# Kernel optimization log

Hardware: AMD Instinct MI355X
Metric: run time of the kernel (lower is better)

## Reference

```python
import jax, jax.numpy as jnp
import numpy as np


def fwht(x):
    """Fast Walsh-Hadamard transform along the last axis (unnormalized)."""
    orig_shape = x.shape
    n = orig_shape[-1]
    x = x.reshape(-1, n)
    h = 1
    while h < n:
        x = x.reshape(-1, n // (2 * h), 2, h)
        a = x[:, :, 0, :]
        b = x[:, :, 1, :]
        x = jnp.stack([a + b, a - b], axis=2).reshape(-1, n)
        h *= 2
    return x.reshape(orig_shape)


def setup_inputs() -> dict:
    key = jax.random.key(0)
    ks = jax.random.split(key, 8)
    M, N = 16384, 4096          # m_pad (out), n_pad (in), powers of 2
    T = 8192
    CB = 65536                  # E8 codebook entries (int16 index space)
    x = jax.random.normal(ks[0], (T, N), dtype=jnp.float32)
    Qidxs = jax.random.randint(ks[1], (M, N // 8), 0, CB, dtype=jnp.int32)
    Qidxs2 = jax.random.randint(ks[2], (M, N // 8), 0, CB, dtype=jnp.int32)
    SU = jnp.where(jax.random.uniform(ks[3], (M,)) < 0.5, -1.0, 1.0).astype(jnp.float32)
    SV = jnp.where(jax.random.uniform(ks[4], (N,)) < 0.5, -1.0, 1.0).astype(jnp.float32)
    codebook = jax.random.normal(ks[5], (CB, 8), dtype=jnp.float32)
    codebook2 = jax.random.normal(ks[6], (CB, 8), dtype=jnp.float32)
    Wscale = jnp.array([0.02], dtype=jnp.float32)
    inv_resid_scale = jnp.array([0.25], dtype=jnp.float32)
    return {"x": x, "Qidxs": Qidxs, "Qidxs2": Qidxs2, "SU": SU, "SV": SV,
            "codebook": codebook, "codebook2": codebook2,
            "Wscale": Wscale, "inv_resid_scale": inv_resid_scale}


def reference(x, Qidxs, Qidxs2, SU, SV, codebook, codebook2, Wscale, inv_resid_scale):
    M = Qidxs.shape[0]
    N = Qidxs.shape[1] * 8
    inv_sqrt_n = 1.0 / np.sqrt(N).astype(np.float32)
    inv_sqrt_m = 1.0 / np.sqrt(M).astype(np.float32)
    # Dequantize RHT-domain weight: 2 residual stages of E8 codebook lookups.
    W_hat = codebook[Qidxs].reshape(M, N)                      # (M, N)
    W_hat = W_hat + inv_resid_scale * codebook2[Qidxs2].reshape(M, N)
    # Input-side RHT: sign flip then normalized Hadamard.
    t = fwht(x * SV) * inv_sqrt_n                              # (T, N)
    # GEMM in the transformed domain.
    z = t @ W_hat.T                                            # (T, M)
    # Output-side RHT: normalized Hadamard, sign flip, global scale.
    y = (fwht(z) * inv_sqrt_m) * SU * Wscale                   # (T, M)
    return y
```

## Files before the change

### kernel.cpp

```cpp
#include <hip/hip_runtime.h>
#include <stdint.h>


typedef __attribute__((ext_vector_type(8)))  __bf16 bf16x8;
typedef __attribute__((ext_vector_type(4)))  float  f32x4;
typedef __attribute__((ext_vector_type(4)))  unsigned short us4;
typedef __attribute__((ext_vector_type(8)))  unsigned short us8;

#define T_ROWS 8192
#define N_DIM  4096
#define M_DIM  16384

__device__ __forceinline__ unsigned short f2bf(float f) {
    unsigned int u = __float_as_uint(f);
    u = (u + 0x7FFFu + ((u >> 16) & 1u)) >> 16;
    return (unsigned short)u;
}
__device__ __forceinline__ float bf2f(unsigned short h) {
    return __uint_as_float(((unsigned int)h) << 16);
}

__device__ __forceinline__ void g2l16(const void* g, void* l) {
    __builtin_amdgcn_global_load_lds(
        (const __attribute__((address_space(1))) void*)g,
        (__attribute__((address_space(3))) void*)l,
        16, 0, 0);
}

__device__ __forceinline__ void fwht16(float v[16]) {
#pragma unroll
    for (int h = 1; h < 16; h <<= 1) {
#pragma unroll
        for (int g = 0; g < 16; g += 2 * h) {
#pragma unroll
            for (int k = 0; k < h; ++k) {
                float a = v[g + k], b = v[g + k + h];
                v[g + k]     = a + b;
                v[g + k + h] = a - b;
            }
        }
    }
}

__device__ __forceinline__ void fwht8(float v[8]) {
#pragma unroll
    for (int h = 1; h < 8; h <<= 1) {
#pragma unroll
        for (int g = 0; g < 8; g += 2 * h) {
#pragma unroll
            for (int k = 0; k < h; ++k) {
                float a = v[g + k], b = v[g + k + h];
                v[g + k]     = a + b;
                v[g + k + h] = a - b;
            }
        }
    }
}

__global__ __launch_bounds__(256) void fwht_x_kernel(
    const float* __restrict__ x, const float* __restrict__ SV,
    unsigned short* __restrict__ t)
{
    __shared__ float s1[16 * 257];
    __shared__ float s2[256 * 17];
    const int row = blockIdx.x;
    const int tid = threadIdx.x;
    float v[16];

    const float4* xv  = (const float4*)(x + (size_t)row * N_DIM + tid * 16);
    const float4* svv = (const float4*)(SV + tid * 16);
#pragma unroll
    for (int q = 0; q < 4; ++q) {
        float4 a = xv[q], b = svv[q];
        v[q*4+0] = a.x*b.x; v[q*4+1] = a.y*b.y;
        v[q*4+2] = a.z*b.z; v[q*4+3] = a.w*b.w;
    }
    fwht16(v);
#pragma unroll
    for (int c = 0; c < 16; ++c) s1[c * 257 + tid] = v[c];
    __syncthreads();

    {
        const int a = tid >> 4, c = tid & 15;
        const float* base = &s1[c * 257 + a * 16];
#pragma unroll
        for (int b = 0; b < 16; ++b) v[b] = base[b];
        fwht16(v);
#pragma unroll
        for (int b = 0; b < 16; ++b) s2[(b * 16 + c) * 17 + a] = v[b];
    }
    __syncthreads();

    {
        const float* base = &s2[tid * 17];
#pragma unroll
        for (int a = 0; a < 16; ++a) v[a] = base[a];
        fwht16(v);
        const float sc = 1.0f / 64.0f;
        unsigned short* out = t + (size_t)row * N_DIM + tid;
#pragma unroll
        for (int a = 0; a < 16; ++a) out[a * 256] = f2bf(v[a] * sc);
    }
}

__device__ __forceinline__ void fwht128_tile(float* __restrict__ s, int tid)
{
#pragma unroll
    for (int k = 0; k < 2; ++k) {
        int sA = tid + k * 256;
        int c = sA & 63, a = sA >> 6;
        float* base = s + c * 129 + a * 16;
        float v[16];
#pragma unroll
        for (int j = 0; j < 16; ++j) v[j] = base[j];
        fwht16(v);
#pragma unroll
        for (int j = 0; j < 16; ++j) base[j] = v[j];
    }
    __syncthreads();
#pragma unroll
    for (int k = 0; k < 4; ++k) {
        int sB = tid + k * 256;
        int c = sB & 63, j = sB >> 6;
        float* base = s + c * 129 + j;
        float v[8];
#pragma unroll
        for (int a = 0; a < 8; ++a) v[a] = base[a * 16];
        fwht8(v);
#pragma unroll
        for (int a = 0; a < 8; ++a) base[a * 16] = v[a];
    }
    __syncthreads();
}

__global__ __launch_bounds__(256) void dec_fwht_kernel(
    const int* __restrict__ Qidxs, const int* __restrict__ Qidxs2,
    const float* __restrict__ cb, const float* __restrict__ cb2,
    const float* __restrict__ inv_resid_scale,
    unsigned short* __restrict__ W)
{
    __shared__ float s[64 * 129];
    const int nt  = blockIdx.x;
    const int grp = blockIdx.y;
    const int tid = threadIdx.x;
    const float irs = inv_resid_scale[0];

#pragma unroll
    for (int k = 0; k < 4; ++k) {
        int slot = tid + k * 256;
        int r = slot >> 3, e = slot & 7;
        size_t m = (size_t)grp * 128 + r;
        size_t q = m * (N_DIM / 8) + nt * 8 + e;
        int i1 = Qidxs[q], i2 = Qidxs2[q];
        const float4* c1 = (const float4*)(cb  + (size_t)i1 * 8);
        const float4* c2 = (const float4*)(cb2 + (size_t)i2 * 8);
        float4 a0 = c1[0], a1 = c1[1], b0 = c2[0], b1 = c2[1];
        float* col = s + (e * 8) * 129 + r;
        col[0 * 129] = a0.x + irs * b0.x;
        col[1 * 129] = a0.y + irs * b0.y;
        col[2 * 129] = a0.z + irs * b0.z;
        col[3 * 129] = a0.w + irs * b0.w;
        col[4 * 129] = a1.x + irs * b1.x;
        col[5 * 129] = a1.y + irs * b1.y;
        col[6 * 129] = a1.z + irs * b1.z;
        col[7 * 129] = a1.w + irs * b1.w;
    }
    __syncthreads();

    fwht128_tile(s, tid);

#pragma unroll
    for (int k = 0; k < 4; ++k) {
        int slot = tid + k * 256;
        int r = slot >> 3, e = slot & 7;
        size_t m = (size_t)grp * 128 + r;
        const float* col = s + (e * 8) * 129 + r;
        us8 o;
#pragma unroll
        for (int j = 0; j < 8; ++j) o[j] = f2bf(col[j * 129]);
        *(us8*)(W + m * N_DIM + nt * 64 + e * 8) = o;
    }
}

__global__ __launch_bounds__(256) void colfwht2_kernel(
    unsigned short* __restrict__ W)
{
    __shared__ float s[64 * 129];
    const int nt  = blockIdx.x;
    const int grp = blockIdx.y;
    const int tid = threadIdx.x;

#pragma unroll
    for (int k = 0; k < 4; ++k) {
        int slot = tid + k * 256;
        int r = slot >> 3, e = slot & 7;
        size_t m = (size_t)grp + (size_t)r * 128;
        us8 v = *(const us8*)(W + m * N_DIM + nt * 64 + e * 8);
        float* col = s + (e * 8) * 129 + r;
#pragma unroll
        for (int j = 0; j < 8; ++j) col[j * 129] = bf2f(v[j]);
    }
    __syncthreads();

    fwht128_tile(s, tid);

    const float sc = 1.0f / 128.0f;
#pragma unroll
    for (int k = 0; k < 4; ++k) {
        int slot = tid + k * 256;
        int r = slot >> 3, e = slot & 7;
        size_t m = (size_t)grp + (size_t)r * 128;
        const float* col = s + (e * 8) * 129 + r;
        us8 o;
#pragma unroll
        for (int j = 0; j < 8; ++j) o[j] = f2bf(col[j * 129] * sc);
        *(us8*)(W + m * N_DIM + nt * 64 + e * 8) = o;
    }
}

__global__ __launch_bounds__(256) void gemm_kernel(
    const unsigned short* __restrict__ A,
    const unsigned short* __restrict__ B,
    const float* __restrict__ SU,
    const float* __restrict__ Wscale,
    float* __restrict__ Y)
{
    __shared__ unsigned short As[128 * 32];
    __shared__ unsigned short Bs[128 * 32];

    const int tid  = threadIdx.x;
    const int lane = tid & 63;
    const int w    = tid >> 6;
    const int wm   = w & 1;
    const int wn   = w >> 1;
    const int i0   = blockIdx.x * 128;
    const int j0   = blockIdx.y * 128;

    f32x4 acc[4][4] = {};

    const int lrow = lane >> 2;
    const int lc8  = (lane & 3) * 8;

    for (int k0 = 0; k0 < N_DIM; k0 += 32) {
        __syncthreads();
#pragma unroll
        for (int q = 0; q < 2; ++q) {
            const int rr = w * 32 + q * 16;
            const unsigned short* ga =
                A + (size_t)(i0 + rr + lrow) * N_DIM + k0 + lc8;
            g2l16(ga, &As[rr * 32]);
            const unsigned short* gb =
                B + (size_t)(j0 + rr + lrow) * N_DIM + k0 + lc8;
            g2l16(gb, &Bs[rr * 32]);
        }
        __syncthreads();

        const int k8   = (lane >> 4) * 8;
        const int mrow = lane & 15;
        bf16x8 af[4], bfr[4];
#pragma unroll
        for (int tm = 0; tm < 4; ++tm)
            af[tm] = *(const bf16x8*)&As[(wm * 64 + tm * 16 + mrow) * 32 + k8];
#pragma unroll
        for (int tn = 0; tn < 4; ++tn)
            bfr[tn] = *(const bf16x8*)&Bs[(wn * 64 + tn * 16 + mrow) * 32 + k8];
#pragma unroll
        for (int tm = 0; tm < 4; ++tm)
#pragma unroll
            for (int tn = 0; tn < 4; ++tn)
                acc[tm][tn] = __builtin_amdgcn_mfma_f32_16x16x32_bf16(
                    af[tm], bfr[tn], acc[tm][tn], 0, 0, 0);
    }

    const float wsc  = Wscale[0];
    const int ccol  = lane & 15;
    const int crow4 = (lane >> 4) * 4;
#pragma unroll
    for (int tn = 0; tn < 4; ++tn) {
        const int col = j0 + wn * 64 + tn * 16 + ccol;
        const float su = SU[col] * wsc;
#pragma unroll
        for (int tm = 0; tm < 4; ++tm) {
            const int rowb = i0 + wm * 64 + tm * 16 + crow4;
#pragma unroll
            for (int r = 0; r < 4; ++r)
                Y[(size_t)(rowb + r) * M_DIM + col] = acc[tm][tn][r] * su;
        }
    }
}

extern "C" void kernel_launch(void* const* d_in, const int* in_sizes, int n_in,
                              void* d_out, int out_size, void* d_ws, size_t ws_size,
                              hipStream_t stream) {
    const float* x       = (const float*)d_in[0];
    const int*   Qidxs   = (const int*)  d_in[1];
    const int*   Qidxs2  = (const int*)  d_in[2];
    const float* SU      = (const float*)d_in[3];
    const float* SV      = (const float*)d_in[4];
    const float* cb      = (const float*)d_in[5];
    const float* cb2     = (const float*)d_in[6];
    const float* Wscale  = (const float*)d_in[7];
    const float* irs     = (const float*)d_in[8];
    float*       y       = (float*)d_out;

    char* ws = (char*)d_ws;
    unsigned short* t  = (unsigned short*)ws;
    unsigned short* W1 = (unsigned short*)(ws + ((size_t)64 << 20));

    fwht_x_kernel<<<T_ROWS, 256, 0, stream>>>(x, SV, t);
    dec_fwht_kernel<<<dim3(N_DIM / 64, M_DIM / 128), 256, 0, stream>>>(
        Qidxs, Qidxs2, cb, cb2, irs, W1);
    colfwht2_kernel<<<dim3(N_DIM / 64, M_DIM / 128), 256, 0, stream>>>(W1);
    gemm_kernel<<<dim3(T_ROWS / 128, M_DIM / 128), 256, 0, stream>>>(
        t, W1, SU, Wscale, y);
}
```

Measured before the change: 2.076 ms.

## Rewrite GEMM as 256x256 tiles with double-buffered swizzled LDS pipeline

Replaces the simple 128x128 GEMM, which reloaded a 32-wide K slice with two syncthreads per step, with a 512-thread 256x256 block tile over 64-wide K tiles. Global-to-LDS loads are double-buffered and issued ahead, with waitcnt-controlled prefetch. LDS uses an XOR swizzle to avoid bank conflicts, and MFMA phases are interleaved with barriers and setprio. The aim is to raise arithmetic intensity and hide memory latency behind the matrix math. The cost is 128KB of LDS per block and many more accumulators per thread, which limits occupancy and adds register pressure.

```diff
diff --git a/kernel.cpp b/kernel.cpp
--- a/kernel.cpp
+++ b/kernel.cpp
@@ -10,6 +10,7 @@
 #define T_ROWS 8192
 #define N_DIM  4096
 #define M_DIM  16384
+#define NT_TILES 64
 
 __device__ __forceinline__ unsigned short f2bf(float f) {
     unsigned int u = __float_as_uint(f);
@@ -218,73 +219,164 @@
     }
 }
 
-__global__ __launch_bounds__(256) void gemm_kernel(
+__global__ __launch_bounds__(512, 2) void gemm_kernel(
     const unsigned short* __restrict__ A,
     const unsigned short* __restrict__ B,
     const float* __restrict__ SU,
     const float* __restrict__ Wscale,
     float* __restrict__ Y)
 {
-    __shared__ unsigned short As[128 * 32];
-    __shared__ unsigned short Bs[128 * 32];
+    __shared__ unsigned short lds[65536];
+    char* ldsc = (char*)lds;
 
     const int tid  = threadIdx.x;
     const int lane = tid & 63;
     const int w    = tid >> 6;
-    const int wm   = w & 1;
-    const int wn   = w >> 1;
-    const int i0   = blockIdx.x * 128;
-    const int j0   = blockIdx.y * 128;
-
-    f32x4 acc[4][4] = {};
-
-    const int lrow = lane >> 2;
-    const int lc8  = (lane & 3) * 8;
-
-    for (int k0 = 0; k0 < N_DIM; k0 += 32) {
-        __syncthreads();
-#pragma unroll
-        for (int q = 0; q < 2; ++q) {
-            const int rr = w * 32 + q * 16;
-            const unsigned short* ga =
-                A + (size_t)(i0 + rr + lrow) * N_DIM + k0 + lc8;
-            g2l16(ga, &As[rr * 32]);
-            const unsigned short* gb =
-                B + (size_t)(j0 + rr + lrow) * N_DIM + k0 + lc8;
-            g2l16(gb, &Bs[rr * 32]);
+    const int wm   = w >> 2;
+    const int wn   = w & 3;
+    const int i0   = blockIdx.x * 256;
+    const int j0   = blockIdx.y * 256;
+
+    const int kgl = lane >> 4;
+    const int lr  = lane & 15;
+    const int rA0 = wm * 128 + lr;
+    const int rB0 = wn * 64  + lr;
+    const int baseA = rA0 * 64 + (kgl ^ ((rA0 >> 1) & 3)) * 16;
+    const int baseB = rB0 * 64 + (kgl ^ ((rB0 >> 1) & 3)) * 16;
+
+    const int G0  = w * 64 + lane;
+    const int G1  = G0 + 512;
+    const int r0g = G0 >> 2, r1g = G1 >> 2;
+    const int kg0 = (G0 & 3) ^ ((r0g >> 1) & 3);
+    const int kg1 = (G1 & 3) ^ ((r1g >> 1) & 3);
+    const unsigned short* Asrc0 = A + (size_t)(i0 + r0g) * N_DIM + kg0 * 8;
+    const unsigned short* Asrc1 = A + (size_t)(i0 + r1g) * N_DIM + kg1 * 8;
+    const unsigned short* Bsrc0 = B + (size_t)(j0 + r0g) * N_DIM + kg0 * 8;
+    const unsigned short* Bsrc1 = B + (size_t)(j0 + r1g) * N_DIM + kg1 * 8;
+    const int ldst0 = G0 * 16 - lane * 16;
+    const int ldst1 = ldst0 + 8192;
+
+    f32x4 acc[8][4] = {};
+
+    g2l16(Asrc0 +  0, ldsc + 0             + ldst0);
+    g2l16(Asrc1 +  0, ldsc + 0             + ldst1);
+    g2l16(Bsrc0 +  0, ldsc + 32768         + ldst0);
+    g2l16(Bsrc1 +  0, ldsc + 32768         + ldst1);
+    g2l16(Asrc0 + 32, ldsc + 16384         + ldst0);
+    g2l16(Asrc1 + 32, ldsc + 16384         + ldst1);
+    g2l16(Bsrc0 + 32, ldsc + 32768 + 16384 + ldst0);
+    g2l16(Bsrc1 + 32, ldsc + 32768 + 16384 + ldst1);
+    g2l16(Asrc0 + 64, ldsc + 65536         + ldst0);
+    g2l16(Asrc1 + 64, ldsc + 65536         + ldst1);
+    g2l16(Bsrc0 + 64, ldsc + 65536 + 32768 + ldst0);
+    g2l16(Bsrc1 + 64, ldsc + 65536 + 32768 + ldst1);
+    asm volatile("s_waitcnt vmcnt(4)" ::: "memory");
+    __builtin_amdgcn_s_barrier();
+
+#pragma unroll 1
+    for (int ktp = 0; ktp < NT_TILES; ktp += 2) {
+#pragma unroll
+        for (int p = 0; p < 2; ++p) {
+            const int  kt  = ktp + p;
+            const int  k0  = kt * 64;
+            const int  sp  = p * 65536;
+            const int  so  = (1 - p) * 65536;
+            const bool st1 = (kt + 1) < NT_TILES;
+            const bool st2 = (kt + 2) < NT_TILES;
+
+            bf16x8 a[8], c[8], b0, b1, b2, b3, d0, d1, d2, d3;
+
+#pragma unroll
+            for (int mf = 0; mf < 8; ++mf)
+                a[mf] = *(const bf16x8*)(ldsc + sp + baseA + mf * 1024);
+            b0 = *(const bf16x8*)(ldsc + sp + 32768 + baseB + 0 * 1024);
+            b1 = *(const bf16x8*)(ldsc + sp + 32768 + baseB + 1 * 1024);
+            if (st1) {
+                g2l16(Asrc0 + k0 + 96, ldsc + so + 16384 + ldst0);
+                g2l16(Asrc1 + k0 + 96, ldsc + so + 16384 + ldst1);
+            }
+            __builtin_amdgcn_s_barrier();
+            __builtin_amdgcn_s_setprio(1);
+#pragma unroll
+            for (int mf = 0; mf < 8; ++mf) {
+                acc[mf][0] = __builtin_amdgcn_mfma_f32_16x16x32_bf16(a[mf], b0, acc[mf][0], 0, 0, 0);
+                acc[mf][1] = __builtin_amdgcn_mfma_f32_16x16x32_bf16(a[mf], b1, acc[mf][1], 0, 0, 0);
+            }
+            __builtin_amdgcn_s_setprio(0);
+            __builtin_amdgcn_s_barrier();
+
+            b2 = *(const bf16x8*)(ldsc + sp + 32768 + baseB + 2 * 1024);
+            b3 = *(const bf16x8*)(ldsc + sp + 32768 + baseB + 3 * 1024);
+#pragma unroll
+            for (int mf = 0; mf < 4; ++mf)
+                c[mf] = *(const bf16x8*)(ldsc + sp + 16384 + baseA + mf * 1024);
+            if (st1) {
+                g2l16(Bsrc0 + k0 + 96, ldsc + so + 32768 + 16384 + ldst0);
+                g2l16(Bsrc1 + k0 + 96, ldsc + so + 32768 + 16384 + ldst1);
+            }
+            __builtin_amdgcn_s_barrier();
+            __builtin_amdgcn_s_setprio(1);
+#pragma unroll
+            for (int mf = 0; mf < 8; ++mf) {
+                acc[mf][2] = __builtin_amdgcn_mfma_f32_16x16x32_bf16(a[mf], b2, acc[mf][2], 0, 0, 0);
+                acc[mf][3] = __builtin_amdgcn_mfma_f32_16x16x32_bf16(a[mf], b3, acc[mf][3], 0, 0, 0);
+            }
+            __builtin_amdgcn_s_setprio(0);
+            __builtin_amdgcn_s_barrier();
+
+#pragma unroll
+            for (int mf = 4; mf < 8; ++mf)
+                c[mf] = *(const bf16x8*)(ldsc + sp + 16384 + baseA + mf * 1024);
+            d0 = *(const bf16x8*)(ldsc + sp + 32768 + 16384 + baseB + 0 * 1024);
+            d1 = *(const bf16x8*)(ldsc + sp + 32768 + 16384 + baseB + 1 * 1024);
+            if (st2) {
+                g2l16(Asrc0 + k0 + 128, ldsc + sp + ldst0);
+                g2l16(Asrc1 + k0 + 128, ldsc + sp + ldst1);
+            }
+            __builtin_amdgcn_s_barrier();
+            __builtin_amdgcn_s_setprio(1);
+#pragma unroll
+            for (int mf = 0; mf < 8; ++mf) {
+                acc[mf][0] = __builtin_amdgcn_mfma_f32_16x16x32_bf16(c[mf], d0, acc[mf][0], 0, 0, 0);
+                acc[mf][1] = __builtin_amdgcn_mfma_f32_16x16x32_bf16(c[mf], d1, acc[mf][1], 0, 0, 0);
+            }
+            __builtin_amdgcn_s_setprio(0);
+            __builtin_amdgcn_s_barrier();
+
+            d2 = *(const bf16x8*)(ldsc + sp + 32768 + 16384 + baseB + 2 * 1024);
+            d3 = *(const bf16x8*)(ldsc + sp + 32768 + 16384 + baseB + 3 * 1024);
+            if (st2) {
+                g2l16(Bsrc0 + k0 + 128, ldsc + sp + 32768 + ldst0);
+                g2l16(Bsrc1 + k0 + 128, ldsc + sp + 32768 + ldst1);
+                asm volatile("s_waitcnt vmcnt(4)" ::: "memory");
+            } else {
+                asm volatile("s_waitcnt vmcnt(0)" ::: "memory");
+            }
+            __builtin_amdgcn_s_barrier();
+            __builtin_amdgcn_s_setprio(1);
+#pragma unroll
+            for (int mf = 0; mf < 8; ++mf) {
+                acc[mf][2] = __builtin_amdgcn_mfma_f32_16x16x32_bf16(c[mf], d2, acc[mf][2], 0, 0, 0);
+                acc[mf][3] = __builtin_amdgcn_mfma_f32_16x16x32_bf16(c[mf], d3, acc[mf][3], 0, 0, 0);
+            }
+            __builtin_amdgcn_s_setprio(0);
+            __builtin_amdgcn_s_barrier();
         }
-        __syncthreads();
-
-        const int k8   = (lane >> 4) * 8;
-        const int mrow = lane & 15;
-        bf16x8 af[4], bfr[4];
-#pragma unroll
-        for (int tm = 0; tm < 4; ++tm)
-            af[tm] = *(const bf16x8*)&As[(wm * 64 + tm * 16 + mrow) * 32 + k8];
-#pragma unroll
-        for (int tn = 0; tn < 4; ++tn)
-            bfr[tn] = *(const bf16x8*)&Bs[(wn * 64 + tn * 16 + mrow) * 32 + k8];
-#pragma unroll
-        for (int tm = 0; tm < 4; ++tm)
-#pragma unroll
-            for (int tn = 0; tn < 4; ++tn)
-                acc[tm][tn] = __builtin_amdgcn_mfma_f32_16x16x32_bf16(
-                    af[tm], bfr[tn], acc[tm][tn], 0, 0, 0);
     }
 
     const float wsc  = Wscale[0];
-    const int ccol  = lane & 15;
-    const int crow4 = (lane >> 4) * 4;
-#pragma unroll
-    for (int tn = 0; tn < 4; ++tn) {
-        const int col = j0 + wn * 64 + tn * 16 + ccol;
+    const int ccol   = lane & 15;
+    const int crow4  = (lane >> 4) * 4;
+#pragma unroll
+    for (int nf = 0; nf < 4; ++nf) {
+        const int col = j0 + wn * 64 + nf * 16 + ccol;
         const float su = SU[col] * wsc;
 #pragma unroll
-        for (int tm = 0; tm < 4; ++tm) {
-            const int rowb = i0 + wm * 64 + tm * 16 + crow4;
+        for (int mf = 0; mf < 8; ++mf) {
+            const int rowb = i0 + wm * 128 + mf * 16 + crow4;
 #pragma unroll
             for (int r = 0; r < 4; ++r)
-                Y[(size_t)(rowb + r) * M_DIM + col] = acc[tm][tn][r] * su;
+                Y[(size_t)(rowb + r) * M_DIM + col] = acc[mf][nf][r] * su;
         }
     }
 }
@@ -311,6 +403,6 @@
     dec_fwht_kernel<<<dim3(N_DIM / 64, M_DIM / 128), 256, 0, stream>>>(
         Qidxs, Qidxs2, cb, cb2, irs, W1);
     colfwht2_kernel<<<dim3(N_DIM / 64, M_DIM / 128), 256, 0, stream>>>(W1);
-    gemm_kernel<<<dim3(T_ROWS / 128, M_DIM / 128), 256, 0, stream>>>(
+    gemm_kernel<<<dim3(T_ROWS / 256, M_DIM / 256), 512, 0, stream>>>(
         t, W1, SU, Wscale, y);
 }
```

New measurement: 1.748 ms. 15.8% less time.
